# Performance work log

Hardware: AMD Instinct MI355X
Metric: run time of the kernel (lower is better)

The kernel has to match this reference:

```python
import jax, jax.numpy as jnp
import numpy as np

D_MODEL = 1024
NUM_HEADS = 16
GROUP_SIZE = 4
NUM_GROUPS = NUM_HEADS // GROUP_SIZE  # 4
D_K = D_MODEL // NUM_HEADS            # 64
THETA = 10000.0
WINDOW = 512


def _rope(x, positions):
    # x: (..., t, d) with d even; interleaved-pair rotation, freq_i = theta^{-i/(d/2)}
    d = x.shape[-1]
    half = d // 2
    inv_freq = THETA ** (-jnp.arange(half, dtype=x.dtype) / half)          # (half,)
    ang = positions.astype(x.dtype)[:, None] * inv_freq[None, :]           # (t, half)
    cos, sin = jnp.cos(ang), jnp.sin(ang)
    x1, x2 = x[..., 0::2], x[..., 1::2]
    r1 = x1 * cos - x2 * sin
    r2 = x1 * sin + x2 * cos
    return jnp.stack([r1, r2], axis=-1).reshape(x.shape)


def setup_inputs() -> dict:
    key = jax.random.key(0)
    k1, k2, k3, k4, k5 = jax.random.split(key, 5)
    b, t = 2, 2048
    scale = 1.0 / np.sqrt(D_MODEL)
    return {
        "x": jax.random.normal(k1, (b, t, D_MODEL), dtype=jnp.float32),
        "WQ": jax.random.normal(k2, (D_MODEL, D_MODEL), dtype=jnp.float32) * scale,
        "WK": jax.random.normal(k3, (NUM_GROUPS * D_K, D_MODEL), dtype=jnp.float32) * scale,
        "WV": jax.random.normal(k4, (NUM_GROUPS * D_K, D_MODEL), dtype=jnp.float32) * scale,
        "WO": jax.random.normal(k5, (D_MODEL, D_MODEL), dtype=jnp.float32) * scale,
        "token_positions": jnp.arange(t, dtype=jnp.int32),
    }


def reference(x, WQ, WK, WV, WO, token_positions):
    b, t, _ = x.shape
    g, s, d = NUM_GROUPS, GROUP_SIZE, D_K
    # projections (Linear: y = x @ W^T, no bias)
    q = (x @ WQ.T).reshape(b, t, g, s, d).transpose(0, 2, 3, 1, 4)  # b g s t d
    k = (x @ WK.T).reshape(b, t, g, d).transpose(0, 2, 1, 3)        # b g t d
    v = (x @ WV.T).reshape(b, t, g, d).transpose(0, 2, 1, 3)        # b g t d
    q = _rope(q, token_positions)
    k = _rope(k, token_positions)
    # scores: kv heads shared across the s query heads of each group
    scores = jnp.einsum('bgsqd,bgkd->bgsqk', q, k) / jnp.sqrt(jnp.asarray(d, x.dtype))
    i = jnp.arange(t)[:, None]
    j = jnp.arange(t)[None, :]
    allowed = (i >= j) & (i - j <= WINDOW)  # causal sliding window
    scores = jnp.where(allowed, scores, -jnp.inf)
    probs = jax.nn.softmax(scores, axis=-1)
    out = jnp.einsum('bgsqk,bgkd->bgsqd', probs, v)                 # b g s t d
    out = out.transpose(0, 3, 1, 2, 4).reshape(b, t, D_MODEL)       # b t (g s d)
    return out @ WO.T
```

## Files before the change

### kernel.cpp

```cpp
#include <hip/hip_runtime.h>
#include <hip/hip_bf16.h>

typedef __bf16 bf16;
typedef __bf16 bf16x8 __attribute__((ext_vector_type(8)));
typedef float  floatx4 __attribute__((ext_vector_type(4)));

#define D_MODEL   1024
#define NUM_HEADS 16
#define NUM_GROUPS 4
#define DK        64
#define SEQ_T     2048
#define BATCH     2
#define M_ROWS    (BATCH*SEQ_T)
#define WINDOW    512
#define KV_DIM    (NUM_GROUPS*DK)
#define N_QKV     (D_MODEL + 2*KV_DIM)
#define QSCALE    0.1803368801111204f
#define FREQ_C    0.4152410118609203f

#define GLDS16(g, l)                                                          \
    __builtin_amdgcn_global_load_lds(                                         \
        (const __attribute__((address_space(1))) void*)(g),                   \
        (__attribute__((address_space(3))) void*)(l), 16, 0, 0)

__global__ __launch_bounds__(256)
void convert_all(const float* s0, bf16* d0, int c0,
                 const float* s1, bf16* d1, int c1,
                 const float* s2, bf16* d2, int c2,
                 const float* s3, bf16* d3, int c3,
                 const float* s4, bf16* d4, int c4)
{
    int id = blockIdx.x * 256 + threadIdx.x;
    const float* src; bf16* dst;
    if      (id < c0)         { src = s0; dst = d0; }
    else if ((id -= c0) < c1) { src = s1; dst = d1; }
    else if ((id -= c1) < c2) { src = s2; dst = d2; }
    else if ((id -= c2) < c3) { src = s3; dst = d3; }
    else if ((id -= c3) < c4) { src = s4; dst = d4; }
    else return;
    int i = id * 8;
    const float* s = src + i;
    float4 a = *(const float4*)s;
    float4 b = *(const float4*)(s + 4);
    bf16x8 v;
    v[0] = (bf16)a.x; v[1] = (bf16)a.y; v[2] = (bf16)a.z; v[3] = (bf16)a.w;
    v[4] = (bf16)b.x; v[5] = (bf16)b.y; v[6] = (bf16)b.z; v[7] = (bf16)b.w;
    *(bf16x8*)&dst[i] = v;
}

__global__ __launch_bounds__(256)
void gemm64(const bf16* __restrict__ A, const bf16* __restrict__ W, int K,
            bf16* __restrict__ Cq, bf16* __restrict__ Ck, bf16* __restrict__ Cv,
            float* __restrict__ Co, const int* __restrict__ pos, int mode, int N)
{
    __shared__ bf16 As0[64 * 32], As1[64 * 32];
    __shared__ bf16 Bs0[128 * 32], Bs1[128 * 32];

    const int tid  = threadIdx.x;
    const int wave = tid >> 6;
    const int lane = tid & 63;
    const int lr   = lane & 15;
    const int quad = lane >> 4;
    const int m0 = blockIdx.y * 64;
    const int n0 = blockIdx.x * 128;
    const int wm = (wave >> 1) * 32;
    const int wn = (wave & 1) * 64;

    const int srow = (lane >> 2);
    const int scol = (lane & 3) * 8;
    const bf16* Ap  = &A[(size_t)(m0 + wave * 16 + srow) * K + scol];
    const bf16* Wp0 = &W[(size_t)(n0 + wave * 16 + srow) * K + scol];
    const bf16* Wp1 = &W[(size_t)(n0 + 64 + wave * 16 + srow) * K + scol];
    bf16* As0d  = &As0[wave * 512];
    bf16* As1d  = &As1[wave * 512];
    bf16* Bs0d0 = &Bs0[wave * 512];
    bf16* Bs0d1 = &Bs0[(wave + 4) * 512];
    bf16* Bs1d0 = &Bs1[wave * 512];
    bf16* Bs1d1 = &Bs1[(wave + 4) * 512];

    floatx4 acc[2][4];
#pragma unroll
    for (int i = 0; i < 2; i++)
#pragma unroll
        for (int j = 0; j < 4; j++) acc[i][j] = (floatx4)(0.0f);

    for (int k0 = 0; k0 < K; k0 += 64) {
        __syncthreads();
        GLDS16(Ap + k0,       As0d);
        GLDS16(Ap + k0 + 32,  As1d);
        GLDS16(Wp0 + k0,      Bs0d0);
        GLDS16(Wp1 + k0,      Bs0d1);
        GLDS16(Wp0 + k0 + 32, Bs1d0);
        GLDS16(Wp1 + k0 + 32, Bs1d1);
        __syncthreads();

        bf16x8 a0[2], a1[2], b0[4], b1[4];
#pragma unroll
        for (int mi = 0; mi < 2; mi++) {
            a0[mi] = *(const bf16x8*)&As0[(wm + mi * 16 + lr) * 32 + quad * 8];
            a1[mi] = *(const bf16x8*)&As1[(wm + mi * 16 + lr) * 32 + quad * 8];
        }
#pragma unroll
        for (int ni = 0; ni < 4; ni++) {
            b0[ni] = *(const bf16x8*)&Bs0[(wn + ni * 16 + lr) * 32 + quad * 8];
            b1[ni] = *(const bf16x8*)&Bs1[(wn + ni * 16 + lr) * 32 + quad * 8];
        }

#pragma unroll
        for (int mi = 0; mi < 2; mi++)
#pragma unroll
            for (int ni = 0; ni < 4; ni++) {
                acc[mi][ni] = __builtin_amdgcn_mfma_f32_16x16x32_bf16(
                    a0[mi], b0[ni], acc[mi][ni], 0, 0, 0);
                acc[mi][ni] = __builtin_amdgcn_mfma_f32_16x16x32_bf16(
                    a1[mi], b1[ni], acc[mi][ni], 0, 0, 0);
            }
    }

    if (mode == 0) {
        bf16* out; int ld, coff;
        if (n0 < D_MODEL)               { out = Cq; ld = D_MODEL; coff = n0; }
        else if (n0 < D_MODEL + KV_DIM) { out = Ck; ld = KV_DIM;  coff = n0 - D_MODEL; }
        else                            { out = Cv; ld = KV_DIM;  coff = n0 - D_MODEL - KV_DIM; }
        const bool rope = (n0 < D_MODEL + KV_DIM);
        const float sc  = (n0 < D_MODEL) ? QSCALE : 1.0f;
        float inv[4];
        float sgn = (lr & 1) ? 1.0f : -1.0f;
        if (rope) {
#pragma unroll
            for (int ni = 0; ni < 4; ni++) {
                int ip = (ni * 16 + lr) >> 1;
                inv[ni] = exp2f(-(float)ip * FREQ_C);
            }
        }
#pragma unroll
        for (int mi = 0; mi < 2; mi++) {
#pragma unroll
            for (int r = 0; r < 4; r++) {
                int row = m0 + wm + mi * 16 + quad * 4 + r;
                float p = rope ? (float)pos[row & (SEQ_T - 1)] : 0.0f;
#pragma unroll
                for (int ni = 0; ni < 4; ni++) {
                    float v = acc[mi][ni][r];
                    if (rope) {
                        float vp = __shfl_xor(v, 1);
                        float ang = p * inv[ni];
                        float ss, cc;
                        __sincosf(ang, &ss, &cc);
                        v = v * cc + vp * ss * sgn;
                    }
                    out[(size_t)row * ld + coff + wn + ni * 16 + lr] = (bf16)(v * sc);
                }
            }
        }
    } else {
#pragma unroll
        for (int mi = 0; mi < 2; mi++)
#pragma unroll
            for (int ni = 0; ni < 4; ni++)
#pragma unroll
                for (int r = 0; r < 4; r++) {
                    int row = m0 + wm + mi * 16 + quad * 4 + r;
                    int col = n0 + wn + ni * 16 + lr;
                    Co[(size_t)row * N + col] = acc[mi][ni][r];
                }
    }
}

__global__ __launch_bounds__(256)
void transpose_v(const bf16* __restrict__ Vw, bf16* __restrict__ Vt)
{
    __shared__ bf16 Ts[64 * 72];
    const int tid = threadIdx.x;
    const int bg = blockIdx.x >> 5;
    const int tt = blockIdx.x & 31;
    const int b = bg >> 2, g = bg & 3;
    const int t0 = tt * 64;

#pragma unroll
    for (int i = 0; i < 2; i++) {
        int c = tid + i * 256;
        int trow = c >> 3, col8 = (c & 7) * 8;
        *(bf16x8*)&Ts[trow * 72 + col8] =
            *(const bf16x8*)&Vw[(size_t)(b * SEQ_T + t0 + trow) * KV_DIM + g * 64 + col8];
    }
    __syncthreads();
#pragma unroll
    for (int i = 0; i < 2; i++) {
        int c = tid + i * 256;
        int drow = c >> 3, tcol8 = (c & 7) * 8;
        bf16x8 v;
#pragma unroll
        for (int j = 0; j < 8; j++) v[j] = Ts[(tcol8 + j) * 72 + drow];
        *(bf16x8*)&Vt[((size_t)(bg * 64 + drow)) * SEQ_T + t0 + tcol8] = v;
    }
}

__global__ __launch_bounds__(256)
void attn_mfma(const bf16* __restrict__ Q, const bf16* __restrict__ K,
               const bf16* __restrict__ Vt_g, bf16* __restrict__ AO)
{
    const int ST = 72;
    __shared__ bf16 Ks[64 * ST];
    __shared__ bf16 Vt[80 * ST];
    __shared__ bf16 Ps[4 * 32 * ST];

    const int tid  = threadIdx.x;
    const int wave = tid >> 6;
    const int lane = tid & 63;
    const int lr   = lane & 15;
    const int quad = lane >> 4;
    const int bg = blockIdx.y;
    const int b = bg >> 2, g = bg & 3;
    const int h = g * 4 + wave;
    const int q0 = blockIdx.x * 32;

    bf16x8 qf[2][2];
#pragma unroll
    for (int mi = 0; mi < 2; mi++)
#pragma unroll
        for (int ks = 0; ks < 2; ks++)
            qf[mi][ks] = *(const bf16x8*)
                &Q[((size_t)(b * SEQ_T + q0 + mi * 16 + lr)) * D_MODEL
                   + h * 64 + ks * 32 + quad * 8];

    for (int i = tid; i < 15 * ST; i += 256) Vt[65 * ST + i] = (bf16)0.0f;
    if (tid < ST) Vt[64 * ST + tid] = (bf16)(tid < 64 ? 1.0f : 0.0f);

    bf16* Pw = &Ps[wave * 32 * ST];

    floatx4 o[2][5];
#pragma unroll
    for (int mi = 0; mi < 2; mi++)
#pragma unroll
        for (int nt = 0; nt < 5; nt++) o[mi][nt] = (floatx4)(0.0f);

    const int t0   = (q0 >= WINDOW) ? ((q0 - WINDOW) & ~63) : 0;
    const int last = q0 & ~63;

    for (int j0 = t0; j0 <= last; j0 += 64) {
        const bool mC = (j0 == last);
        const bool mW = (q0 >= WINDOW) && (j0 == t0);
        __syncthreads();
#pragma unroll
        for (int i = 0; i < 2; i++) {
            int c = tid + i * 256;
            int row = c >> 3, col8 = (c & 7) * 8;
            *(bf16x8*)&Ks[row * ST + col8] =
                *(const bf16x8*)&K[((size_t)(b * SEQ_T + j0 + row)) * KV_DIM + g * 64 + col8];
            *(bf16x8*)&Vt[row * ST + col8] =
                *(const bf16x8*)&Vt_g[((size_t)(bg * 64 + row)) * SEQ_T + j0 + col8];
        }
        __syncthreads();

        floatx4 s[2][4];
#pragma unroll
        for (int mi = 0; mi < 2; mi++)
#pragma unroll
            for (int nt = 0; nt < 4; nt++) s[mi][nt] = (floatx4)(0.0f);
#pragma unroll
        for (int ks = 0; ks < 2; ks++) {
#pragma unroll
            for (int nt = 0; nt < 4; nt++) {
                bf16x8 kf = *(const bf16x8*)&Ks[(nt * 16 + lr) * ST + ks * 32 + quad * 8];
                s[0][nt] = __builtin_amdgcn_mfma_f32_16x16x32_bf16(qf[0][ks], kf, s[0][nt], 0, 0, 0);
                s[1][nt] = __builtin_amdgcn_mfma_f32_16x16x32_bf16(qf[1][ks], kf, s[1][nt], 0, 0, 0);
            }
        }

        if (mC) {
#pragma unroll
            for (int mi = 0; mi < 2; mi++)
#pragma unroll
                for (int nt = 0; nt < 4; nt++) {
                    int key = j0 + nt * 16 + lr;
#pragma unroll
                    for (int r = 0; r < 4; r++) {
                        int qi_ = q0 + mi * 16 + quad * 4 + r;
                        s[mi][nt][r] = (key <= qi_) ? s[mi][nt][r] : -1e30f;
                    }
                }
        } else if (mW) {
#pragma unroll
            for (int mi = 0; mi < 2; mi++)
#pragma unroll
                for (int nt = 0; nt < 4; nt++) {
                    int key = j0 + nt * 16 + lr;
#pragma unroll
                    for (int r = 0; r < 4; r++) {
                        int qi_ = q0 + mi * 16 + quad * 4 + r;
                        s[mi][nt][r] = (qi_ - key <= WINDOW) ? s[mi][nt][r] : -1e30f;
                    }
                }
        }

#pragma unroll
        for (int mi = 0; mi < 2; mi++)
#pragma unroll
            for (int nt = 0; nt < 4; nt++)
#pragma unroll
                for (int r = 0; r < 4; r++)
                    Pw[(mi * 16 + quad * 4 + r) * ST + nt * 16 + lr] =
                        (bf16)exp2f(s[mi][nt][r]);

        __asm__ volatile("s_waitcnt lgkmcnt(0)" ::: "memory");

#pragma unroll
        for (int ks = 0; ks < 2; ks++) {
            bf16x8 pf0 = *(const bf16x8*)&Pw[(0 + lr) * ST + ks * 32 + quad * 8];
            bf16x8 pf1 = *(const bf16x8*)&Pw[(16 + lr) * ST + ks * 32 + quad * 8];
#pragma unroll
            for (int nt = 0; nt < 5; nt++) {
                bf16x8 vf = *(const bf16x8*)&Vt[(nt * 16 + lr) * ST + ks * 32 + quad * 8];
                o[0][nt] = __builtin_amdgcn_mfma_f32_16x16x32_bf16(pf0, vf, o[0][nt], 0, 0, 0);
                o[1][nt] = __builtin_amdgcn_mfma_f32_16x16x32_bf16(pf1, vf, o[1][nt], 0, 0, 0);
            }
        }
    }

#pragma unroll
    for (int mi = 0; mi < 2; mi++)
#pragma unroll
        for (int r = 0; r < 4; r++) {
            float l = __shfl(o[mi][4][r], lane & 48);
            float invl = 1.0f / l;
            int row = q0 + mi * 16 + quad * 4 + r;
#pragma unroll
            for (int nt = 0; nt < 4; nt++)
                AO[((size_t)(b * SEQ_T + row)) * D_MODEL + h * 64 + nt * 16 + lr] =
                    (bf16)(o[mi][nt][r] * invl);
        }
}

extern "C" void kernel_launch(void* const* d_in, const int* in_sizes, int n_in,
                              void* d_out, int out_size, void* d_ws, size_t ws_size,
                              hipStream_t stream)
{
    const float* x  = (const float*)d_in[0];
    const float* WQ = (const float*)d_in[1];
    const float* WK = (const float*)d_in[2];
    const float* WV = (const float*)d_in[3];
    const float* WO = (const float*)d_in[4];
    const int*  pos = (const int*)d_in[5];

    char* ws   = (char*)d_ws;
    bf16* Qw   = (bf16*)ws;
    bf16* Kw   = (bf16*)(ws + (size_t) 8 * 1024 * 1024);
    bf16* Vw   = (bf16*)(ws + (size_t)10 * 1024 * 1024);
    bf16* xb   = (bf16*)(ws + (size_t)12 * 1024 * 1024);
    bf16* AO   = xb;
    bf16* Wqkv = (bf16*)(ws + (size_t)20 * 1024 * 1024);
    bf16* Vt_g = Wqkv;
    bf16* WOb  = (bf16*)(ws + (size_t)23 * 1024 * 1024);

    const int cx = (M_ROWS * D_MODEL) / 8;
    const int cq = (D_MODEL * D_MODEL) / 8;
    const int ck = (KV_DIM * D_MODEL) / 8;
    const int ctot = cx + cq + 2 * ck + cq;
    convert_all<<<ctot / 256, 256, 0, stream>>>(
        x, xb, cx,
        WQ, Wqkv, cq,
        WK, Wqkv + (size_t)D_MODEL * D_MODEL, ck,
        WV, Wqkv + (size_t)(D_MODEL + KV_DIM) * D_MODEL, ck,
        WO, WOb, cq);

    gemm64<<<dim3(N_QKV / 128, M_ROWS / 64), 256, 0, stream>>>(
        xb, Wqkv, D_MODEL, Qw, Kw, Vw, nullptr, pos, 0, N_QKV);

    transpose_v<<<256, 256, 0, stream>>>(Vw, Vt_g);

    attn_mfma<<<dim3(SEQ_T / 32, BATCH * NUM_GROUPS), 256, 0, stream>>>(
        Qw, Kw, Vt_g, AO);

    gemm64<<<dim3(D_MODEL / 128, M_ROWS / 64), 256, 0, stream>>>(
        AO, WOb, D_MODEL, nullptr, nullptr, nullptr, (float*)d_out, pos, 1, D_MODEL);
}
```

Measured before the change: 155.5 us.

## Fuse V transpose into QKV GEMM epilogue and shrink GEMM tile to 64x64

```diff
diff --git a/kernel.cpp b/kernel.cpp
--- a/kernel.cpp
+++ b/kernel.cpp
@@ -2,6 +2,7 @@
 #include <hip/hip_bf16.h>
 
 typedef __bf16 bf16;
+typedef __bf16 bf16x4 __attribute__((ext_vector_type(4)));
 typedef __bf16 bf16x8 __attribute__((ext_vector_type(8)));
 typedef float  floatx4 __attribute__((ext_vector_type(4)));
 
@@ -48,13 +49,13 @@
     *(bf16x8*)&dst[i] = v;
 }
 
-__global__ __launch_bounds__(256)
-void gemm64(const bf16* __restrict__ A, const bf16* __restrict__ W, int K,
-            bf16* __restrict__ Cq, bf16* __restrict__ Ck, bf16* __restrict__ Cv,
-            float* __restrict__ Co, const int* __restrict__ pos, int mode, int N)
+__global__ __launch_bounds__(256, 6)
+void gemm_t64(const bf16* __restrict__ A, const bf16* __restrict__ W, int K,
+              bf16* __restrict__ Cq, bf16* __restrict__ Ck, bf16* __restrict__ Vt,
+              float* __restrict__ Co, const int* __restrict__ pos, int mode)
 {
     __shared__ bf16 As0[64 * 32], As1[64 * 32];
-    __shared__ bf16 Bs0[128 * 32], Bs1[128 * 32];
+    __shared__ bf16 Bs0[64 * 32], Bs1[64 * 32];
 
     const int tid  = threadIdx.x;
     const int wave = tid >> 6;
@@ -62,46 +63,41 @@
     const int lr   = lane & 15;
     const int quad = lane >> 4;
     const int m0 = blockIdx.y * 64;
-    const int n0 = blockIdx.x * 128;
+    const int n0 = blockIdx.x * 64;
     const int wm = (wave >> 1) * 32;
-    const int wn = (wave & 1) * 64;
+    const int wn = (wave & 1) * 32;
 
     const int srow = (lane >> 2);
     const int scol = (lane & 3) * 8;
-    const bf16* Ap  = &A[(size_t)(m0 + wave * 16 + srow) * K + scol];
-    const bf16* Wp0 = &W[(size_t)(n0 + wave * 16 + srow) * K + scol];
-    const bf16* Wp1 = &W[(size_t)(n0 + 64 + wave * 16 + srow) * K + scol];
-    bf16* As0d  = &As0[wave * 512];
-    bf16* As1d  = &As1[wave * 512];
-    bf16* Bs0d0 = &Bs0[wave * 512];
-    bf16* Bs0d1 = &Bs0[(wave + 4) * 512];
-    bf16* Bs1d0 = &Bs1[wave * 512];
-    bf16* Bs1d1 = &Bs1[(wave + 4) * 512];
-
-    floatx4 acc[2][4];
+    const bf16* Ap = &A[(size_t)(m0 + wave * 16 + srow) * K + scol];
+    const bf16* Wp = &W[(size_t)(n0 + wave * 16 + srow) * K + scol];
+    bf16* As0d = &As0[wave * 512];
+    bf16* As1d = &As1[wave * 512];
+    bf16* Bs0d = &Bs0[wave * 512];
+    bf16* Bs1d = &Bs1[wave * 512];
+
+    floatx4 acc[2][2];
 #pragma unroll
     for (int i = 0; i < 2; i++)
 #pragma unroll
-        for (int j = 0; j < 4; j++) acc[i][j] = (floatx4)(0.0f);
+        for (int j = 0; j < 2; j++) acc[i][j] = (floatx4)(0.0f);
 
     for (int k0 = 0; k0 < K; k0 += 64) {
         __syncthreads();
-        GLDS16(Ap + k0,       As0d);
-        GLDS16(Ap + k0 + 32,  As1d);
-        GLDS16(Wp0 + k0,      Bs0d0);
-        GLDS16(Wp1 + k0,      Bs0d1);
-        GLDS16(Wp0 + k0 + 32, Bs1d0);
-        GLDS16(Wp1 + k0 + 32, Bs1d1);
+        GLDS16(Ap + k0,      As0d);
+        GLDS16(Ap + k0 + 32, As1d);
+        GLDS16(Wp + k0,      Bs0d);
+        GLDS16(Wp + k0 + 32, Bs1d);
         __syncthreads();
 
-        bf16x8 a0[2], a1[2], b0[4], b1[4];
+        bf16x8 a0[2], a1[2], b0[2], b1[2];
 #pragma unroll
         for (int mi = 0; mi < 2; mi++) {
             a0[mi] = *(const bf16x8*)&As0[(wm + mi * 16 + lr) * 32 + quad * 8];
             a1[mi] = *(const bf16x8*)&As1[(wm + mi * 16 + lr) * 32 + quad * 8];
         }
 #pragma unroll
-        for (int ni = 0; ni < 4; ni++) {
+        for (int ni = 0; ni < 2; ni++) {
             b0[ni] = *(const bf16x8*)&Bs0[(wn + ni * 16 + lr) * 32 + quad * 8];
             b1[ni] = *(const bf16x8*)&Bs1[(wn + ni * 16 + lr) * 32 + quad * 8];
         }
@@ -109,7 +105,7 @@
 #pragma unroll
         for (int mi = 0; mi < 2; mi++)
 #pragma unroll
-            for (int ni = 0; ni < 4; ni++) {
+            for (int ni = 0; ni < 2; ni++) {
                 acc[mi][ni] = __builtin_amdgcn_mfma_f32_16x16x32_bf16(
                     a0[mi], b0[ni], acc[mi][ni], 0, 0, 0);
                 acc[mi][ni] = __builtin_amdgcn_mfma_f32_16x16x32_bf16(
@@ -118,38 +114,49 @@
     }
 
     if (mode == 0) {
-        bf16* out; int ld, coff;
-        if (n0 < D_MODEL)               { out = Cq; ld = D_MODEL; coff = n0; }
-        else if (n0 < D_MODEL + KV_DIM) { out = Ck; ld = KV_DIM;  coff = n0 - D_MODEL; }
-        else                            { out = Cv; ld = KV_DIM;  coff = n0 - D_MODEL - KV_DIM; }
-        const bool rope = (n0 < D_MODEL + KV_DIM);
-        const float sc  = (n0 < D_MODEL) ? QSCALE : 1.0f;
-        float inv[4];
-        float sgn = (lr & 1) ? 1.0f : -1.0f;
-        if (rope) {
-#pragma unroll
-            for (int ni = 0; ni < 4; ni++) {
-                int ip = (ni * 16 + lr) >> 1;
+        if (n0 >= D_MODEL + KV_DIM) {
+            const int g  = (n0 - (D_MODEL + KV_DIM)) >> 6;
+            const int b  = m0 >> 11;
+            const int bg = b * 4 + g;
+#pragma unroll
+            for (int mi = 0; mi < 2; mi++) {
+#pragma unroll
+                for (int ni = 0; ni < 2; ni++) {
+                    int d  = wn + ni * 16 + lr;
+                    int t0 = (m0 & (SEQ_T - 1)) + wm + mi * 16 + quad * 4;
+                    bf16x4 v;
+#pragma unroll
+                    for (int r = 0; r < 4; r++) v[r] = (bf16)acc[mi][ni][r];
+                    *(bf16x4*)&Vt[((size_t)(bg * 64 + d)) * SEQ_T + t0] = v;
+                }
+            }
+        } else {
+            bf16* out; int ld, coff; float sc;
+            if (n0 < D_MODEL) { out = Cq; ld = D_MODEL; coff = n0; sc = QSCALE; }
+            else              { out = Ck; ld = KV_DIM;  coff = n0 - D_MODEL; sc = 1.0f; }
+            float inv[2];
+            float sgn = (lr & 1) ? 1.0f : -1.0f;
+#pragma unroll
+            for (int ni = 0; ni < 2; ni++) {
+                int ip = (wn + ni * 16 + lr) >> 1;
                 inv[ni] = exp2f(-(float)ip * FREQ_C);
             }
-        }
-#pragma unroll
-        for (int mi = 0; mi < 2; mi++) {
-#pragma unroll
-            for (int r = 0; r < 4; r++) {
-                int row = m0 + wm + mi * 16 + quad * 4 + r;
-                float p = rope ? (float)pos[row & (SEQ_T - 1)] : 0.0f;
-#pragma unroll
-                for (int ni = 0; ni < 4; ni++) {
-                    float v = acc[mi][ni][r];
-                    if (rope) {
+#pragma unroll
+            for (int mi = 0; mi < 2; mi++) {
+#pragma unroll
+                for (int r = 0; r < 4; r++) {
+                    int row = m0 + wm + mi * 16 + quad * 4 + r;
+                    float p = (float)pos[row & (SEQ_T - 1)];
+#pragma unroll
+                    for (int ni = 0; ni < 2; ni++) {
+                        float v  = acc[mi][ni][r];
                         float vp = __shfl_xor(v, 1);
                         float ang = p * inv[ni];
                         float ss, cc;
                         __sincosf(ang, &ss, &cc);
                         v = v * cc + vp * ss * sgn;
+                        out[(size_t)row * ld + coff + wn + ni * 16 + lr] = (bf16)(v * sc);
                     }
-                    out[(size_t)row * ld + coff + wn + ni * 16 + lr] = (bf16)(v * sc);
                 }
             }
         }
@@ -157,42 +164,13 @@
 #pragma unroll
         for (int mi = 0; mi < 2; mi++)
 #pragma unroll
-            for (int ni = 0; ni < 4; ni++)
+            for (int ni = 0; ni < 2; ni++)
 #pragma unroll
                 for (int r = 0; r < 4; r++) {
                     int row = m0 + wm + mi * 16 + quad * 4 + r;
                     int col = n0 + wn + ni * 16 + lr;
-                    Co[(size_t)row * N + col] = acc[mi][ni][r];
-                }
-    }
-}
-
-__global__ __launch_bounds__(256)
-void transpose_v(const bf16* __restrict__ Vw, bf16* __restrict__ Vt)
-{
-    __shared__ bf16 Ts[64 * 72];
-    const int tid = threadIdx.x;
-    const int bg = blockIdx.x >> 5;
-    const int tt = blockIdx.x & 31;
-    const int b = bg >> 2, g = bg & 3;
-    const int t0 = tt * 64;
-
-#pragma unroll
-    for (int i = 0; i < 2; i++) {
-        int c = tid + i * 256;
-        int trow = c >> 3, col8 = (c & 7) * 8;
-        *(bf16x8*)&Ts[trow * 72 + col8] =
-            *(const bf16x8*)&Vw[(size_t)(b * SEQ_T + t0 + trow) * KV_DIM + g * 64 + col8];
-    }
-    __syncthreads();
-#pragma unroll
-    for (int i = 0; i < 2; i++) {
-        int c = tid + i * 256;
-        int drow = c >> 3, tcol8 = (c & 7) * 8;
-        bf16x8 v;
-#pragma unroll
-        for (int j = 0; j < 8; j++) v[j] = Ts[(tcol8 + j) * 72 + drow];
-        *(bf16x8*)&Vt[((size_t)(bg * 64 + drow)) * SEQ_T + t0 + tcol8] = v;
+                    Co[(size_t)row * D_MODEL + col] = acc[mi][ni][r];
+                }
     }
 }
 
@@ -346,11 +324,10 @@
     char* ws   = (char*)d_ws;
     bf16* Qw   = (bf16*)ws;
     bf16* Kw   = (bf16*)(ws + (size_t) 8 * 1024 * 1024);
-    bf16* Vw   = (bf16*)(ws + (size_t)10 * 1024 * 1024);
+    bf16* Vt_g = (bf16*)(ws + (size_t)10 * 1024 * 1024);
     bf16* xb   = (bf16*)(ws + (size_t)12 * 1024 * 1024);
     bf16* AO   = xb;
     bf16* Wqkv = (bf16*)(ws + (size_t)20 * 1024 * 1024);
-    bf16* Vt_g = Wqkv;
     bf16* WOb  = (bf16*)(ws + (size_t)23 * 1024 * 1024);
 
     const int cx = (M_ROWS * D_MODEL) / 8;
@@ -364,14 +341,12 @@
         WV, Wqkv + (size_t)(D_MODEL + KV_DIM) * D_MODEL, ck,
         WO, WOb, cq);
 
-    gemm64<<<dim3(N_QKV / 128, M_ROWS / 64), 256, 0, stream>>>(
-        xb, Wqkv, D_MODEL, Qw, Kw, Vw, nullptr, pos, 0, N_QKV);
-
-    transpose_v<<<256, 256, 0, stream>>>(Vw, Vt_g);
+    gemm_t64<<<dim3(N_QKV / 64, M_ROWS / 64), 256, 0, stream>>>(
+        xb, Wqkv, D_MODEL, Qw, Kw, Vt_g, nullptr, pos, 0);
 
     attn_mfma<<<dim3(SEQ_T / 32, BATCH * NUM_GROUPS), 256, 0, stream>>>(
         Qw, Kw, Vt_g, AO);
 
-    gemm64<<<dim3(D_MODEL / 128, M_ROWS / 64), 256, 0, stream>>>(
-        AO, WOb, D_MODEL, nullptr, nullptr, nullptr, (float*)d_out, pos, 1, D_MODEL);
+    gemm_t64<<<dim3(D_MODEL / 64, M_ROWS / 64), 256, 0, stream>>>(
+        AO, WOb, D_MODEL, nullptr, nullptr, nullptr, (float*)d_out, pos, 1);
 }
```

Result: faster. 151.4 us, median of 2 (-2.6%).
